# Kernel tuning notes

Hardware: AMD Instinct MI355X
Metric: run time of the kernel (lower is better)

The kernel has to match this reference:

```python
import jax, jax.numpy as jnp
from jax import lax
import numpy as np

B, N, C = 4, 16384, 64
M_POINT, K_SAMPLE = 1024, 32
RADIUS = 0.5
LN_EPS = 1e-5
CP = C + 3  # grouped channels with use_xyz


def _fps(xyz, m):
    """D-FPS: furthest point sampling on Euclidean coords. xyz (B,N,3) -> (B,m) int32."""
    b, n, _ = xyz.shape
    min_d = jnp.full((b, n), 1e10, xyz.dtype)
    pt0 = xyz[:, 0]  # CUDA FPS starts from index 0

    def step(carry, _):
        md, last = carry
        d = jnp.sum((xyz - last[:, None, :]) ** 2, axis=-1)  # (B,N)
        md = jnp.minimum(md, d)
        idx = jnp.argmax(md, axis=1)  # (B,)
        nxt = jnp.take_along_axis(xyz, idx[:, None, None], axis=1)[:, 0]
        return (md, nxt), idx.astype(jnp.int32)

    _, idxs = lax.scan(step, (min_d, pt0), None, length=m - 1)  # (m-1,B)
    return jnp.concatenate([jnp.zeros((1, b), jnp.int32), idxs], axis=0).T  # (B,m)


def _ball_query(xyz, new_xyz, radius, k):
    """First k neighbors (by original index) within radius; pad with first hit. -> (B,M,k)."""
    b, n, _ = xyz.shape
    d2 = jnp.sum((new_xyz[:, :, None, :] - xyz[:, None, :, :]) ** 2, -1)  # (B,M,N)
    scores = jnp.where(d2 <= radius * radius, jnp.arange(n, dtype=jnp.int32), n)
    neg_top, _ = lax.top_k(-scores, k)  # k smallest scores = first k in-radius indices
    idx = -neg_top  # (B,M,k), ascending
    idx = jnp.where(idx < n, idx, idx[..., :1])  # pad invalid slots with first hit
    return idx


def setup_inputs() -> dict:
    key = jax.random.key(0)
    ks = jax.random.split(key, 8)
    points_xyz = jax.random.uniform(ks[0], (B, N, 3)) * 2.0 - 1.0
    features = jax.random.normal(ks[1], (B, C, N))
    prompt_emb = jax.random.normal(ks[2], (1, M_POINT, 2)) * 0.02
    proj_w = jax.random.normal(ks[3], (CP, 2)) * 0.5
    proj_b = jnp.zeros((CP,))
    ln_g = jnp.ones((CP,))
    ln_b = jnp.zeros((CP,))
    pw_w = jax.random.normal(ks[4], (M_POINT, CP)) * 0.05
    pw_b = jnp.zeros((M_POINT,))
    w0 = jax.random.normal(ks[5], (128, CP)) / np.sqrt(CP)
    b0 = jnp.zeros((128,))
    w1 = jax.random.normal(ks[6], (256, 128)) / np.sqrt(128.0)
    b1 = jnp.zeros((256,))
    return dict(points_xyz=points_xyz, features=features, prompt_emb=prompt_emb,
                proj_w=proj_w, proj_b=proj_b, ln_g=ln_g, ln_b=ln_b,
                pw_w=pw_w, pw_b=pw_b, w0=w0, b0=b0, w1=w1, b1=b1)


def reference(points_xyz, features, prompt_emb, proj_w, proj_b, ln_g, ln_b,
              pw_w, pw_b, w0, b0, w1, b1):
    # sample centers (D-FPS)
    indices = _fps(points_xyz, M_POINT)                                   # (B,M)
    new_xyz = jnp.take_along_axis(points_xyz, indices[:, :, None], axis=1)  # (B,M,3)
    # ball-query grouping + gather
    idx = _ball_query(points_xyz, new_xyz, RADIUS, K_SAMPLE)              # (B,M,K)
    gx = jax.vmap(lambda p, i: p[i])(points_xyz, idx)                     # (B,M,K,3)
    gx = gx - new_xyz[:, :, None, :]                                      # relative xyz
    gf = jax.vmap(lambda f, i: f[:, i])(features, idx)                    # (B,C,M,K)
    g = jnp.concatenate([jnp.transpose(gx, (0, 3, 1, 2)), gf], axis=1)    # (B,C+3,M,K)
    # incorporate_prompt
    emb = g.mean(axis=(-2, -1))                                           # (B,C+3)
    pw = jax.nn.softmax(emb @ pw_w.T + pw_b, axis=1)                      # (B,M)
    pe = prompt_emb @ proj_w.T + proj_b                                   # (1,M,C+3)
    mu = pe.mean(-1, keepdims=True)
    var = ((pe - mu) ** 2).mean(-1, keepdims=True)
    pe = (pe - mu) * lax.rsqrt(var + LN_EPS) * ln_g + ln_b
    pe = jax.nn.gelu(pe, approximate=False)                               # (1,M,C+3)
    g = g + pe[0].T[None, :, :, None] * pw[:, None, :, None]              # (B,C+3,M,K)
    # shared MLP (1x1 conv) + ReLU
    h = jax.nn.relu(jnp.einsum('oc,bcmk->bomk', w0, g) + b0[:, None, None])
    h = jax.nn.relu(jnp.einsum('oc,bcmk->bomk', w1, h) + b1[:, None, None])
    # max pool over neighbors K
    pooled = h.max(axis=-1)                                               # (B,256,M)
    return new_xyz, pooled, indices
```

## Files before the change

kernel.cpp:

```cpp
#include <hip/hip_runtime.h>
#include <hip/hip_bf16.h>

#define NB   4
#define NPTS 16384
#define NC   64
#define NM   1024
#define NK   32
#define NCP  67
#define RAD2 0.25f

#define OFF_W0T     0u
#define OFF_W1T     8576u
#define OFF_NEWXYZ  41344u
#define OFF_IDXBALL 53632u
#define OFF_CNT     184704u
#define OFF_EMB     250240u
#define OFF_PW      250624u
#define OFF_PE      254720u
#define OFF_SX      323328u
#define OFF_SY      388864u
#define OFF_SZ      454400u
#define OFF_SKLO    519936u

#define OUT_NEWXYZ 0u
#define OUT_POOLED 12288u
#define OUT_IDX    1060864u

__global__ __launch_bounds__(256) void k_prepw(const float* __restrict__ w0,
                                               const float* __restrict__ w1,
                                               float* __restrict__ w0t,
                                               float* __restrict__ w1t) {
  int t = blockIdx.x * 256 + threadIdx.x;
  if (t < 128 * NCP) { int o = t / NCP, c = t % NCP; w0t[c * 128 + o] = w0[t]; }
  if (t < 256 * 128) { int o2 = t / 128, o = t % 128; w1t[o * 256 + o2] = w1[t]; }
}

__device__ __forceinline__ unsigned mpart3(unsigned v) {
  return (v & 1u) | ((v & 2u) << 2) | ((v & 4u) << 4);
}
__device__ __forceinline__ unsigned cellof(float x, float y, float z) {
  unsigned qx = (unsigned)fminf(fmaxf((x + 1.0f) * 4.0f, 0.0f), 7.0f);
  unsigned qy = (unsigned)fminf(fmaxf((y + 1.0f) * 4.0f, 0.0f), 7.0f);
  unsigned qz = (unsigned)fminf(fmaxf((z + 1.0f) * 4.0f, 0.0f), 7.0f);
  return mpart3(qx) | (mpart3(qy) << 1) | (mpart3(qz) << 2);
}

__global__ __launch_bounds__(1024) void k_sort(const float* __restrict__ xyz,
                                               float* __restrict__ sx,
                                               float* __restrict__ sy,
                                               float* __restrict__ sz,
                                               unsigned* __restrict__ sklo) {
  const int b = blockIdx.x, t = threadIdx.x;
  const int lane = t & 63, wid = t >> 6;
  const float* xb = xyz + (size_t)b * NPTS * 3;
  __shared__ unsigned s_hist[512], s_off[512], s_wsum[8];
  if (t < 512) s_hist[t] = 0u;
  __syncthreads();
#pragma unroll
  for (int i = 0; i < 16; ++i) {
    int p = t + 1024 * i;
    float x = xb[p * 3 + 0], y = xb[p * 3 + 1], z = xb[p * 3 + 2];
    atomicAdd(&s_hist[cellof(x, y, z)], 1u);
  }
  __syncthreads();
  unsigned v = (t < 512) ? s_hist[t] : 0u;
#pragma unroll
  for (int off = 1; off < 64; off <<= 1) {
    unsigned u = __shfl_up(v, off);
    if (lane >= off) v += u;
  }
  if (t < 512 && lane == 63) s_wsum[wid] = v;
  __syncthreads();
  if (t < 512) {
    unsigned add = 0;
    for (int w = 0; w < wid; ++w) add += s_wsum[w];
    s_off[t] = add + v - s_hist[t];
  }
  __syncthreads();
#pragma unroll
  for (int i = 0; i < 16; ++i) {
    int p = t + 1024 * i;
    float x = xb[p * 3 + 0], y = xb[p * 3 + 1], z = xb[p * 3 + 2];
    unsigned pos = atomicAdd(&s_off[cellof(x, y, z)], 1u);
    sx[b * NPTS + pos] = x;
    sy[b * NPTS + pos] = y;
    sz[b * NPTS + pos] = z;
    sklo[b * NPTS + pos] = 16383u - (unsigned)p;
  }
}

__device__ __forceinline__ unsigned long long umax64(unsigned long long a,
                                                     unsigned long long b) {
  return a > b ? a : b;
}

__global__ __launch_bounds__(1024) void k_fps(const float* __restrict__ xyz,
                                              const float* __restrict__ sx,
                                              const float* __restrict__ sy,
                                              const float* __restrict__ sz,
                                              const unsigned* __restrict__ sklo,
                                              float* __restrict__ newxyz,
                                              float* __restrict__ out) {
  const int b = blockIdx.x, t = threadIdx.x;
  const int lane = t & 63, wid = t >> 6;
  const float* xb = xyz + (size_t)b * NPTS * 3;
  const float* bx = sx + b * NPTS;
  const float* by_ = sy + b * NPTS;
  const float* bz_ = sz + b * NPTS;
  const unsigned* bk = sklo + b * NPTS;
  __shared__ float s_md[NPTS];
  __shared__ unsigned short s_klo[NPTS];
  __shared__ float s_bbox[256][6];
  __shared__ unsigned long long s_bkey[256];
  __shared__ int s_list[2][256];
  __shared__ int s_cnt[2];
#pragma unroll
  for (int i = 0; i < 16; ++i) {
    int p = t + 1024 * i;
    s_md[p] = 1e10f;
    s_klo[p] = (unsigned short)bk[p];
  }
  if (t < 256) s_bkey[t] = ((unsigned long long)__float_as_uint(1e10f)) << 32;
  if (t < 2) s_cnt[t] = 0;
  for (int bb = wid; bb < 256; bb += 16) {
    int p = bb * 64 + lane;
    float x = bx[p], y = by_[p], z = bz_[p];
    float xl = x, xh = x, yl = y, yh = y, zl = z, zh = z;
#pragma unroll
    for (int off = 1; off < 64; off <<= 1) {
      xl = fminf(xl, __shfl_xor(xl, off)); xh = fmaxf(xh, __shfl_xor(xh, off));
      yl = fminf(yl, __shfl_xor(yl, off)); yh = fmaxf(yh, __shfl_xor(yh, off));
      zl = fminf(zl, __shfl_xor(zl, off)); zh = fmaxf(zh, __shfl_xor(zh, off));
    }
    if (lane == 0) {
      s_bbox[bb][0] = xl; s_bbox[bb][1] = xh;
      s_bbox[bb][2] = yl; s_bbox[bb][3] = yh;
      s_bbox[bb][4] = zl; s_bbox[bb][5] = zh;
    }
  }
  float lx = xb[0], ly = xb[1], lz = xb[2];
  if (t == 0) {
    newxyz[(size_t)b * NM * 3 + 0] = lx;
    newxyz[(size_t)b * NM * 3 + 1] = ly;
    newxyz[(size_t)b * NM * 3 + 2] = lz;
    out[OUT_NEWXYZ + (size_t)b * NM * 3 + 0] = lx;
    out[OUT_NEWXYZ + (size_t)b * NM * 3 + 1] = ly;
    out[OUT_NEWXYZ + (size_t)b * NM * 3 + 2] = lz;
    out[OUT_IDX + b * NM] = 0.0f;
  }
  __syncthreads();
  for (int s = 1; s < NM; ++s) {
    const int pp = s & 1;
    if (t == 256) s_cnt[pp ^ 1] = 0;
    if (t < 256) {
      float mm = __uint_as_float((unsigned)(s_bkey[t] >> 32));
      float gx = fmaxf(fmaxf(__fsub_rn(s_bbox[t][0], lx), __fsub_rn(lx, s_bbox[t][1])), 0.0f);
      float gy = fmaxf(fmaxf(__fsub_rn(s_bbox[t][2], ly), __fsub_rn(ly, s_bbox[t][3])), 0.0f);
      float gz = fmaxf(fmaxf(__fsub_rn(s_bbox[t][4], lz), __fsub_rn(lz, s_bbox[t][5])), 0.0f);
      float lb = __fadd_rn(__fadd_rn(__fmul_rn(gx, gx), __fmul_rn(gy, gy)),
                           __fmul_rn(gz, gz));
      if (!(lb * 0.999984741f > mm * 1.000015259f)) {
        int pos = atomicAdd(&s_cnt[pp], 1);
        s_list[pp][pos] = t;
      }
    }
    __syncthreads();
    const int nb = s_cnt[pp];
    for (int w = wid; w < nb; w += 16) {
      int bb = s_list[pp][w];
      int p = bb * 64 + lane;
      float dx = __fsub_rn(bx[p], lx);
      float dy = __fsub_rn(by_[p], ly);
      float dz = __fsub_rn(bz_[p], lz);
      float d2 = __fadd_rn(__fadd_rn(__fmul_rn(dx, dx), __fmul_rn(dy, dy)),
                           __fmul_rn(dz, dz));
      float m0 = fminf(s_md[p], d2);
      s_md[p] = m0;
      unsigned long long key =
          (((unsigned long long)__float_as_uint(m0)) << 32) |
          (unsigned long long)s_klo[p];
#pragma unroll
      for (int off = 1; off < 64; off <<= 1) {
        unsigned long long o = __shfl_xor(key, off);
        key = o > key ? o : key;
      }
      if (lane == 0) s_bkey[bb] = key;
    }
    __syncthreads();
    unsigned long long k =
        umax64(umax64(s_bkey[lane], s_bkey[lane + 64]),
               umax64(s_bkey[lane + 128], s_bkey[lane + 192]));
#pragma unroll
    for (int off = 1; off < 64; off <<= 1) {
      unsigned long long o = __shfl_xor(k, off);
      k = o > k ? o : k;
    }
    const int bi = 16383 - (int)(unsigned)(k & 0xffffffffull);
    lx = xb[bi * 3 + 0];
    ly = xb[bi * 3 + 1];
    lz = xb[bi * 3 + 2];
    if (t == 0) {
      newxyz[((size_t)b * NM + s) * 3 + 0] = lx;
      newxyz[((size_t)b * NM + s) * 3 + 1] = ly;
      newxyz[((size_t)b * NM + s) * 3 + 2] = lz;
      out[OUT_NEWXYZ + ((size_t)b * NM + s) * 3 + 0] = lx;
      out[OUT_NEWXYZ + ((size_t)b * NM + s) * 3 + 1] = ly;
      out[OUT_NEWXYZ + ((size_t)b * NM + s) * 3 + 2] = lz;
      out[OUT_IDX + b * NM + s] = (float)bi;
    }
  }
}

__global__ __launch_bounds__(256) void k_ball(const float* __restrict__ xyz,
                                              const float* __restrict__ newxyz,
                                              int* __restrict__ idxball,
                                              int* __restrict__ cnt,
                                              float* __restrict__ emb) {
  __shared__ int s_idx[4][NK];
  const int lane = threadIdx.x & 63, wid = threadIdx.x >> 6;
  const int gid = blockIdx.x * 4 + wid;
  const int b = gid >> 10;
  const float* xb = xyz + (size_t)b * NPTS * 3;
  const float cx = newxyz[gid * 3 + 0];
  const float cy = newxyz[gid * 3 + 1];
  const float cz = newxyz[gid * 3 + 2];
  int total = 0;
  for (int base = 0; base < NPTS && total < NK; base += 64) {
    int n = base + lane;
    float dx = __fsub_rn(xb[n * 3 + 0], cx);
    float dy = __fsub_rn(xb[n * 3 + 1], cy);
    float dz = __fsub_rn(xb[n * 3 + 2], cz);
    float d2 = __fadd_rn(__fadd_rn(__fmul_rn(dx, dx), __fmul_rn(dy, dy)),
                         __fmul_rn(dz, dz));
    bool hit = d2 <= RAD2;
    unsigned long long mask = __ballot(hit);
    int pos = total + (int)__popcll(mask & ((1ull << lane) - 1ull));
    if (hit && pos < NK) s_idx[wid][pos] = n;
    total += (int)__popcll(mask);
  }
  int tt = total < NK ? total : NK;
  if (lane >= tt && lane < NK) s_idx[wid][lane] = s_idx[wid][0];
  int v = 0;
  if (lane < NK) {
    v = s_idx[wid][lane];
    idxball[(size_t)gid * NK + lane] = v;
    atomicAdd(&cnt[b * NPTS + v], 1);
  }
  float sx = 0.f, sy = 0.f, sz = 0.f;
  if (lane < NK) { sx = xb[v * 3 + 0]; sy = xb[v * 3 + 1]; sz = xb[v * 3 + 2]; }
#pragma unroll
  for (int off = 1; off < 64; off <<= 1) {
    sx += __shfl_xor(sx, off);
    sy += __shfl_xor(sy, off);
    sz += __shfl_xor(sz, off);
  }
  if (lane == 0) {
    atomicAdd(&emb[b * 96 + 0], sx - 32.0f * cx);
    atomicAdd(&emb[b * 96 + 1], sy - 32.0f * cy);
    atomicAdd(&emb[b * 96 + 2], sz - 32.0f * cz);
  }
}

__global__ __launch_bounds__(256) void k_embfeat(const float* __restrict__ feat,
                                                 const int* __restrict__ cnt,
                                                 float* __restrict__ emb) {
  const int c = blockIdx.x, b = blockIdx.y;
  const float* f = feat + ((size_t)b * NC + c) * NPTS;
  const int* ct = cnt + b * NPTS;
  float acc = 0.f;
  for (int n = threadIdx.x; n < NPTS; n += 256)
    acc = fmaf((float)ct[n], f[n], acc);
  __shared__ float red[4];
#pragma unroll
  for (int off = 1; off < 64; off <<= 1) acc += __shfl_xor(acc, off);
  if ((threadIdx.x & 63) == 0) red[threadIdx.x >> 6] = acc;
  __syncthreads();
  if (threadIdx.x == 0)
    emb[b * 96 + 3 + c] = red[0] + red[1] + red[2] + red[3];
}

__global__ __launch_bounds__(64) void k_pe(const float* __restrict__ prompt,
                                           const float* __restrict__ projw,
                                           const float* __restrict__ projb,
                                           const float* __restrict__ lng,
                                           const float* __restrict__ lnb,
                                           float* __restrict__ pe) {
  const int m = blockIdx.x, lane = threadIdx.x;
  const float p0 = prompt[m * 2 + 0], p1 = prompt[m * 2 + 1];
  const int c1 = lane, c2 = lane + 64;
  float v1 = p0 * projw[c1 * 2 + 0] + p1 * projw[c1 * 2 + 1] + projb[c1];
  float v2 = 0.f;
  if (c2 < NCP) v2 = p0 * projw[c2 * 2 + 0] + p1 * projw[c2 * 2 + 1] + projb[c2];
  float s = v1 + ((c2 < NCP) ? v2 : 0.f);
#pragma unroll
  for (int off = 1; off < 64; off <<= 1) s += __shfl_xor(s, off);
  float mu = s * (1.0f / 67.0f);
  float d1 = v1 - mu;
  float d2v = (c2 < NCP) ? (v2 - mu) : 0.f;
  float q = d1 * d1 + d2v * d2v;
#pragma unroll
  for (int off = 1; off < 64; off <<= 1) q += __shfl_xor(q, off);
  float inv = 1.0f / sqrtf(q * (1.0f / 67.0f) + 1e-5f);
  {
    float y = d1 * inv * lng[c1] + lnb[c1];
    pe[m * NCP + c1] = 0.5f * y * (1.0f + erff(y * 0.70710678118654752f));
  }
  if (c2 < NCP) {
    float y = (v2 - mu) * inv * lng[c2] + lnb[c2];
    pe[m * NCP + c2] = 0.5f * y * (1.0f + erff(y * 0.70710678118654752f));
  }
}

__global__ __launch_bounds__(1024) void k_pw(const float* __restrict__ emb,
                                             const float* __restrict__ pww,
                                             const float* __restrict__ pwb,
                                             float* __restrict__ pw) {
  const int b = blockIdx.x, m = threadIdx.x;
  __shared__ float se[NCP];
  __shared__ float red[16];
  __shared__ float bcast;
  if (m < NCP) se[m] = emb[b * 96 + m] * (1.0f / 32768.0f);
  __syncthreads();
  float acc = pwb[m];
  for (int c = 0; c < NCP; ++c) acc = fmaf(se[c], pww[m * NCP + c], acc);
  float mx = acc;
#pragma unroll
  for (int off = 1; off < 64; off <<= 1) mx = fmaxf(mx, __shfl_xor(mx, off));
  if ((m & 63) == 0) red[m >> 6] = mx;
  __syncthreads();
  if (m == 0) {
    float v = red[0];
    for (int w = 1; w < 16; ++w) v = fmaxf(v, red[w]);
    bcast = v;
  }
  __syncthreads();
  float e = expf(acc - bcast);
  float ssum = e;
#pragma unroll
  for (int off = 1; off < 64; off <<= 1) ssum += __shfl_xor(ssum, off);
  if ((m & 63) == 0) red[m >> 6] = ssum;
  __syncthreads();
  if (m == 0) {
    float v = 0.f;
    for (int w = 0; w < 16; ++w) v += red[w];
    bcast = v;
  }
  __syncthreads();
  pw[b * NM + m] = e / bcast;
}

__global__ __launch_bounds__(256) void k_main(const float* __restrict__ feat,
                                              const float* __restrict__ xyz,
                                              const float* __restrict__ newxyz,
                                              const int* __restrict__ idxball,
                                              const float* __restrict__ pe,
                                              const float* __restrict__ pwbuf,
                                              const float* __restrict__ w0t,
                                              const float* __restrict__ b0,
                                              const float* __restrict__ w1t,
                                              const float* __restrict__ b1,
                                              float* __restrict__ out) {
  __shared__ __align__(16) float g[NCP * 36];
  __shared__ __align__(16) float h0[128 * 36];
  __shared__ int s_idx[NK];
  __shared__ float spe[NCP];
  const int bid = blockIdx.x;
  const int b = bid >> 10, m = bid & 1023;
  const int t = threadIdx.x;
  const float pwv = pwbuf[bid];
  if (t < NK) {
    int n = idxball[(size_t)bid * NK + t];
    n = n < 0 ? 0 : (n > NPTS - 1 ? NPTS - 1 : n);
    s_idx[t] = n;
  }
  if (t < NCP) spe[t] = pe[m * NCP + t] * pwv;
  __syncthreads();
  for (int e = t; e < NK * NC; e += 256) {
    int k = e >> 6, c = e & 63;
    int n = s_idx[k];
    g[(3 + c) * 36 + k] = feat[((size_t)b * NC + c) * NPTS + n] + spe[3 + c];
  }
  if (t < 96) {
    int k = t & 31, d = t >> 5;
    int n = s_idx[k];
    float cv = newxyz[bid * 3 + d];
    g[d * 36 + k] = (xyz[((size_t)b * NPTS + n) * 3 + d] - cv) + spe[d];
  }
  __syncthreads();
  {
    const int o = t & 127, kb = (t >> 7) * 16;
    float acc[16];
    float bb = b0[o];
#pragma unroll
    for (int j = 0; j < 16; ++j) acc[j] = bb;
    for (int c = 0; c < NCP; ++c) {
      float w = w0t[c * 128 + o];
      const float4* gp = reinterpret_cast<const float4*>(&g[c * 36 + kb]);
#pragma unroll
      for (int qq = 0; qq < 4; ++qq) {
        float4 gv = gp[qq];
        acc[qq * 4 + 0] = fmaf(w, gv.x, acc[qq * 4 + 0]);
        acc[qq * 4 + 1] = fmaf(w, gv.y, acc[qq * 4 + 1]);
        acc[qq * 4 + 2] = fmaf(w, gv.z, acc[qq * 4 + 2]);
        acc[qq * 4 + 3] = fmaf(w, gv.w, acc[qq * 4 + 3]);
      }
    }
    float4* hp = reinterpret_cast<float4*>(&h0[o * 36 + kb]);
#pragma unroll
    for (int qq = 0; qq < 4; ++qq) {
      float4 hv;
      hv.x = fmaxf(acc[qq * 4 + 0], 0.f);
      hv.y = fmaxf(acc[qq * 4 + 1], 0.f);
      hv.z = fmaxf(acc[qq * 4 + 2], 0.f);
      hv.w = fmaxf(acc[qq * 4 + 3], 0.f);
      hp[qq] = hv;
    }
  }
  __syncthreads();
  {
    const int o2 = t;
    float acc[32];
    float bb = b1[o2];
#pragma unroll
    for (int j = 0; j < 32; ++j) acc[j] = bb;
    for (int o = 0; o < 128; ++o) {
      float w = w1t[o * 256 + o2];
      const float4* hp = reinterpret_cast<const float4*>(&h0[o * 36]);
#pragma unroll
      for (int qq = 0; qq < 8; ++qq) {
        float4 hv = hp[qq];
        acc[qq * 4 + 0] = fmaf(w, hv.x, acc[qq * 4 + 0]);
        acc[qq * 4 + 1] = fmaf(w, hv.y, acc[qq * 4 + 1]);
        acc[qq * 4 + 2] = fmaf(w, hv.z, acc[qq * 4 + 2]);
        acc[qq * 4 + 3] = fmaf(w, hv.w, acc[qq * 4 + 3]);
      }
    }
    float mx = 0.f;
#pragma unroll
    for (int k = 0; k < 32; ++k) mx = fmaxf(mx, acc[k]);
    out[OUT_POOLED + ((size_t)(b * 256 + o2)) * NM + m] = mx;
  }
}

extern "C" void kernel_launch(void* const* d_in, const int* in_sizes, int n_in,
                              void* d_out, int out_size, void* d_ws, size_t ws_size,
                              hipStream_t stream) {
  const float* xyz    = (const float*)d_in[0];
  const float* feat   = (const float*)d_in[1];
  const float* prompt = (const float*)d_in[2];
  const float* projw  = (const float*)d_in[3];
  const float* projb  = (const float*)d_in[4];
  const float* lng    = (const float*)d_in[5];
  const float* lnb    = (const float*)d_in[6];
  const float* pww    = (const float*)d_in[7];
  const float* pwb    = (const float*)d_in[8];
  const float* w0     = (const float*)d_in[9];
  const float* b0     = (const float*)d_in[10];
  const float* w1     = (const float*)d_in[11];
  const float* b1     = (const float*)d_in[12];
  float* ws = (float*)d_ws;
  float* out = (float*)d_out;

  float* w0t      = ws + OFF_W0T;
  float* w1t      = ws + OFF_W1T;
  float* nxyz     = ws + OFF_NEWXYZ;
  int*   idxball  = (int*)(ws + OFF_IDXBALL);
  int*   cnt      = (int*)(ws + OFF_CNT);
  float* emb      = ws + OFF_EMB;
  float* pwv      = ws + OFF_PW;
  float* pev      = ws + OFF_PE;
  float* sxw      = ws + OFF_SX;
  float* syw      = ws + OFF_SY;
  float* szw      = ws + OFF_SZ;
  unsigned* sklo  = (unsigned*)(ws + OFF_SKLO);

  hipMemsetAsync(cnt, 0, NB * NPTS * sizeof(int), stream);
  hipMemsetAsync(emb, 0, NB * 96 * sizeof(float), stream);

  k_prepw<<<128, 256, 0, stream>>>(w0, w1, w0t, w1t);
  k_sort<<<NB, 1024, 0, stream>>>(xyz, sxw, syw, szw, sklo);
  k_fps<<<NB, 1024, 0, stream>>>(xyz, sxw, syw, szw, sklo, nxyz, out);
  k_ball<<<NB * NM / 4, 256, 0, stream>>>(xyz, nxyz, idxball, cnt, emb);
  k_embfeat<<<dim3(NC, NB), 256, 0, stream>>>(feat, cnt, emb);
  k_pe<<<NM, 64, 0, stream>>>(prompt, projw, projb, lng, lnb, pev);
  k_pw<<<NB, 1024, 0, stream>>>(emb, pww, pwb, pwv);
  k_main<<<NB * NM, 256, 0, stream>>>(feat, xyz, nxyz, idxball, pev, pwv,
                                      w0t, b0, w1t, b1, out);
}
```

Before: 2.248 ms.

## Restructure FPS loop: one barrier per step, per-wave bucket ownership, cached winner coords

```diff
diff --git a/kernel.cpp b/kernel.cpp
--- a/kernel.cpp
+++ b/kernel.cpp
@@ -93,51 +93,123 @@
                                                      unsigned long long b) {
   return a > b ? a : b;
 }
-
-__global__ __launch_bounds__(1024) void k_fps(const float* __restrict__ xyz,
-                                              const float* __restrict__ sx,
-                                              const float* __restrict__ sy,
-                                              const float* __restrict__ sz,
-                                              const unsigned* __restrict__ sklo,
-                                              float* __restrict__ newxyz,
-                                              float* __restrict__ out) {
+__device__ __forceinline__ unsigned long long pack_key(float m, unsigned kl,
+                                                       int bb) {
+  return (((unsigned long long)__float_as_uint(m)) << 22) |
+         (((unsigned long long)kl) << 8) | (unsigned long long)(unsigned)bb;
+}
+
+template <bool INIT>
+__device__ __forceinline__ void fps_bucket(
+    int bbp, int gl, float lx, float ly, float lz,
+    const float* __restrict__ bx, const float* __restrict__ by,
+    const float* __restrict__ bz, const unsigned* __restrict__ bk,
+    float* s_md, unsigned short* s_klo,
+    unsigned long long* skey_out, float4* swin_out,
+    float* s_bxl, float* s_bxh, float* s_byl, float* s_byh,
+    float* s_bzl, float* s_bzh) {
+  const int p0 = bbp * 64 + gl * 8;
+  float4 xa = *(const float4*)(bx + p0);
+  float4 xc = *(const float4*)(bx + p0 + 4);
+  float4 ya = *(const float4*)(by + p0);
+  float4 yc = *(const float4*)(by + p0 + 4);
+  float4 za = *(const float4*)(bz + p0);
+  float4 zc = *(const float4*)(bz + p0 + 4);
+  float xx[8] = {xa.x, xa.y, xa.z, xa.w, xc.x, xc.y, xc.z, xc.w};
+  float yy[8] = {ya.x, ya.y, ya.z, ya.w, yc.x, yc.y, yc.z, yc.w};
+  float zz[8] = {za.x, za.y, za.z, za.w, zc.x, zc.y, zc.z, zc.w};
+  unsigned kls[8];
+  float mds[8];
+  if constexpr (INIT) {
+    uint4 k0 = *(const uint4*)(bk + p0);
+    uint4 k1 = *(const uint4*)(bk + p0 + 4);
+    kls[0] = k0.x; kls[1] = k0.y; kls[2] = k0.z; kls[3] = k0.w;
+    kls[4] = k1.x; kls[5] = k1.y; kls[6] = k1.z; kls[7] = k1.w;
+  } else {
+    uint4 kv = *(const uint4*)(&s_klo[p0]);
+    kls[0] = kv.x & 0xFFFFu; kls[1] = kv.x >> 16;
+    kls[2] = kv.y & 0xFFFFu; kls[3] = kv.y >> 16;
+    kls[4] = kv.z & 0xFFFFu; kls[5] = kv.z >> 16;
+    kls[6] = kv.w & 0xFFFFu; kls[7] = kv.w >> 16;
+    float4 ma = *(const float4*)(&s_md[p0]);
+    float4 mb = *(const float4*)(&s_md[p0 + 4]);
+    mds[0] = ma.x; mds[1] = ma.y; mds[2] = ma.z; mds[3] = ma.w;
+    mds[4] = mb.x; mds[5] = mb.y; mds[6] = mb.z; mds[7] = mb.w;
+  }
+  unsigned long long best = 0ull;
+  float bwx = 0.f, bwy = 0.f, bwz = 0.f;
+  float nmd[8];
+#pragma unroll
+  for (int i = 0; i < 8; ++i) {
+    float dx = __fsub_rn(xx[i], lx);
+    float dy = __fsub_rn(yy[i], ly);
+    float dz = __fsub_rn(zz[i], lz);
+    float d2 = __fadd_rn(__fadd_rn(__fmul_rn(dx, dx), __fmul_rn(dy, dy)),
+                         __fmul_rn(dz, dz));
+    float m = INIT ? d2 : fminf(mds[i], d2);
+    nmd[i] = m;
+    unsigned long long key = pack_key(m, kls[i], bbp);
+    if (key > best) { best = key; bwx = xx[i]; bwy = yy[i]; bwz = zz[i]; }
+  }
+  *(float4*)(&s_md[p0])     = make_float4(nmd[0], nmd[1], nmd[2], nmd[3]);
+  *(float4*)(&s_md[p0 + 4]) = make_float4(nmd[4], nmd[5], nmd[6], nmd[7]);
+  if constexpr (INIT) {
+    uint4 kw;
+    kw.x = kls[0] | (kls[1] << 16); kw.y = kls[2] | (kls[3] << 16);
+    kw.z = kls[4] | (kls[5] << 16); kw.w = kls[6] | (kls[7] << 16);
+    *(uint4*)(&s_klo[p0]) = kw;
+  }
+  unsigned long long gk = best;
+#pragma unroll
+  for (int off = 1; off < 8; off <<= 1) {
+    unsigned long long o = __shfl_xor(gk, off);
+    gk = o > gk ? o : gk;
+  }
+  if constexpr (INIT) {
+    float xl = xx[0], xh = xx[0], yl = yy[0], yh = yy[0], zl = zz[0], zh = zz[0];
+#pragma unroll
+    for (int i = 1; i < 8; ++i) {
+      xl = fminf(xl, xx[i]); xh = fmaxf(xh, xx[i]);
+      yl = fminf(yl, yy[i]); yh = fmaxf(yh, yy[i]);
+      zl = fminf(zl, zz[i]); zh = fmaxf(zh, zz[i]);
+    }
+#pragma unroll
+    for (int off = 1; off < 8; off <<= 1) {
+      xl = fminf(xl, __shfl_xor(xl, off)); xh = fmaxf(xh, __shfl_xor(xh, off));
+      yl = fminf(yl, __shfl_xor(yl, off)); yh = fmaxf(yh, __shfl_xor(yh, off));
+      zl = fminf(zl, __shfl_xor(zl, off)); zh = fmaxf(zh, __shfl_xor(zh, off));
+    }
+    if (gl == 0) {
+      s_bxl[bbp] = xl; s_bxh[bbp] = xh;
+      s_byl[bbp] = yl; s_byh[bbp] = yh;
+      s_bzl[bbp] = zl; s_bzh[bbp] = zh;
+    }
+  }
+  if (best == gk) swin_out[bbp] = make_float4(bwx, bwy, bwz, 0.f);
+  if (gl == 0) skey_out[bbp] = gk;
+}
+
+__global__ __launch_bounds__(512) void k_fps(const float* __restrict__ xyz,
+                                             const float* __restrict__ sx,
+                                             const float* __restrict__ sy,
+                                             const float* __restrict__ sz,
+                                             const unsigned* __restrict__ sklo,
+                                             float* __restrict__ newxyz,
+                                             float* __restrict__ out) {
   const int b = blockIdx.x, t = threadIdx.x;
-  const int lane = t & 63, wid = t >> 6;
+  const int lane = t & 63, w = t >> 6;
+  const int gl = lane & 7, g = lane >> 3;
   const float* xb = xyz + (size_t)b * NPTS * 3;
   const float* bx = sx + b * NPTS;
-  const float* by_ = sy + b * NPTS;
-  const float* bz_ = sz + b * NPTS;
+  const float* by = sy + b * NPTS;
+  const float* bz = sz + b * NPTS;
   const unsigned* bk = sklo + b * NPTS;
   __shared__ float s_md[NPTS];
   __shared__ unsigned short s_klo[NPTS];
-  __shared__ float s_bbox[256][6];
-  __shared__ unsigned long long s_bkey[256];
-  __shared__ int s_list[2][256];
-  __shared__ int s_cnt[2];
-#pragma unroll
-  for (int i = 0; i < 16; ++i) {
-    int p = t + 1024 * i;
-    s_md[p] = 1e10f;
-    s_klo[p] = (unsigned short)bk[p];
-  }
-  if (t < 256) s_bkey[t] = ((unsigned long long)__float_as_uint(1e10f)) << 32;
-  if (t < 2) s_cnt[t] = 0;
-  for (int bb = wid; bb < 256; bb += 16) {
-    int p = bb * 64 + lane;
-    float x = bx[p], y = by_[p], z = bz_[p];
-    float xl = x, xh = x, yl = y, yh = y, zl = z, zh = z;
-#pragma unroll
-    for (int off = 1; off < 64; off <<= 1) {
-      xl = fminf(xl, __shfl_xor(xl, off)); xh = fmaxf(xh, __shfl_xor(xh, off));
-      yl = fminf(yl, __shfl_xor(yl, off)); yh = fmaxf(yh, __shfl_xor(yh, off));
-      zl = fminf(zl, __shfl_xor(zl, off)); zh = fmaxf(zh, __shfl_xor(zh, off));
-    }
-    if (lane == 0) {
-      s_bbox[bb][0] = xl; s_bbox[bb][1] = xh;
-      s_bbox[bb][2] = yl; s_bbox[bb][3] = yh;
-      s_bbox[bb][4] = zl; s_bbox[bb][5] = zh;
-    }
-  }
+  __shared__ float s_bxl[256], s_bxh[256], s_byl[256], s_byh[256],
+                   s_bzl[256], s_bzh[256];
+  __shared__ unsigned long long s_bkey[2][256];
+  __shared__ float4 s_bwin[2][256];
   float lx = xb[0], ly = xb[1], lz = xb[2];
   if (t == 0) {
     newxyz[(size_t)b * NM * 3 + 0] = lx;
@@ -148,66 +220,68 @@
     out[OUT_NEWXYZ + (size_t)b * NM * 3 + 2] = lz;
     out[OUT_IDX + b * NM] = 0.0f;
   }
+#pragma unroll
+  for (int r = 0; r < 4; ++r) {
+    int bbp = 32 * w + r * 8 + g;
+    fps_bucket<true>(bbp, gl, lx, ly, lz, bx, by, bz, bk, s_md, s_klo,
+                     s_bkey[0], s_bwin[0],
+                     s_bxl, s_bxh, s_byl, s_byh, s_bzl, s_bzh);
+  }
   __syncthreads();
   for (int s = 1; s < NM; ++s) {
-    const int pp = s & 1;
-    if (t == 256) s_cnt[pp ^ 1] = 0;
-    if (t < 256) {
-      float mm = __uint_as_float((unsigned)(s_bkey[t] >> 32));
-      float gx = fmaxf(fmaxf(__fsub_rn(s_bbox[t][0], lx), __fsub_rn(lx, s_bbox[t][1])), 0.0f);
-      float gy = fmaxf(fmaxf(__fsub_rn(s_bbox[t][2], ly), __fsub_rn(ly, s_bbox[t][3])), 0.0f);
-      float gz = fmaxf(fmaxf(__fsub_rn(s_bbox[t][4], lz), __fsub_rn(lz, s_bbox[t][5])), 0.0f);
-      float lb = __fadd_rn(__fadd_rn(__fmul_rn(gx, gx), __fmul_rn(gy, gy)),
-                           __fmul_rn(gz, gz));
-      if (!(lb * 0.999984741f > mm * 1.000015259f)) {
-        int pos = atomicAdd(&s_cnt[pp], 1);
-        s_list[pp][pos] = t;
-      }
-    }
-    __syncthreads();
-    const int nb = s_cnt[pp];
-    for (int w = wid; w < nb; w += 16) {
-      int bb = s_list[pp][w];
-      int p = bb * 64 + lane;
-      float dx = __fsub_rn(bx[p], lx);
-      float dy = __fsub_rn(by_[p], ly);
-      float dz = __fsub_rn(bz_[p], lz);
-      float d2 = __fadd_rn(__fadd_rn(__fmul_rn(dx, dx), __fmul_rn(dy, dy)),
-                           __fmul_rn(dz, dz));
-      float m0 = fminf(s_md[p], d2);
-      s_md[p] = m0;
-      unsigned long long key =
-          (((unsigned long long)__float_as_uint(m0)) << 32) |
-          (unsigned long long)s_klo[p];
-#pragma unroll
-      for (int off = 1; off < 64; off <<= 1) {
-        unsigned long long o = __shfl_xor(key, off);
-        key = o > key ? o : key;
-      }
-      if (lane == 0) s_bkey[bb] = key;
-    }
-    __syncthreads();
+    const int cur = s & 1, prv = cur ^ 1;
     unsigned long long k =
-        umax64(umax64(s_bkey[lane], s_bkey[lane + 64]),
-               umax64(s_bkey[lane + 128], s_bkey[lane + 192]));
+        umax64(umax64(s_bkey[prv][lane], s_bkey[prv][lane + 64]),
+               umax64(s_bkey[prv][lane + 128], s_bkey[prv][lane + 192]));
 #pragma unroll
     for (int off = 1; off < 64; off <<= 1) {
       unsigned long long o = __shfl_xor(k, off);
       k = o > k ? o : k;
     }
-    const int bi = 16383 - (int)(unsigned)(k & 0xffffffffull);
-    lx = xb[bi * 3 + 0];
-    ly = xb[bi * 3 + 1];
-    lz = xb[bi * 3 + 2];
+    const int bbw = (int)(k & 0xFFull);
+    float4 wv = s_bwin[prv][bbw];
+    lx = wv.x; ly = wv.y; lz = wv.z;
     if (t == 0) {
+      const int idx = 16383 - (int)((k >> 8) & 0x3FFFull);
       newxyz[((size_t)b * NM + s) * 3 + 0] = lx;
       newxyz[((size_t)b * NM + s) * 3 + 1] = ly;
       newxyz[((size_t)b * NM + s) * 3 + 2] = lz;
       out[OUT_NEWXYZ + ((size_t)b * NM + s) * 3 + 0] = lx;
       out[OUT_NEWXYZ + ((size_t)b * NM + s) * 3 + 1] = ly;
       out[OUT_NEWXYZ + ((size_t)b * NM + s) * 3 + 2] = lz;
-      out[OUT_IDX + b * NM + s] = (float)bi;
-    }
+      out[OUT_IDX + b * NM + s] = (float)idx;
+    }
+    bool keep = false;
+    if (lane < 32) {
+      const int bbj = 32 * w + lane;
+      unsigned long long kj = s_bkey[prv][bbj];
+      float mm = __uint_as_float((unsigned)(kj >> 22));
+      float gx = fmaxf(fmaxf(__fsub_rn(s_bxl[bbj], lx), __fsub_rn(lx, s_bxh[bbj])), 0.f);
+      float gy = fmaxf(fmaxf(__fsub_rn(s_byl[bbj], ly), __fsub_rn(ly, s_byh[bbj])), 0.f);
+      float gz = fmaxf(fmaxf(__fsub_rn(s_bzl[bbj], lz), __fsub_rn(lz, s_bzh[bbj])), 0.f);
+      float lb = __fadd_rn(__fadd_rn(__fmul_rn(gx, gx), __fmul_rn(gy, gy)),
+                           __fmul_rn(gz, gz));
+      keep = !(__fmul_rn(lb, 0.999984741f) > __fmul_rn(mm, 1.000015259f));
+      if (!keep) {
+        s_bkey[cur][bbj] = kj;
+        s_bwin[cur][bbj] = s_bwin[prv][bbj];
+      }
+    }
+    unsigned long long mask = __ballot(keep);
+    while (mask) {
+      unsigned long long m2 = mask;
+#pragma unroll
+      for (int r = 0; r < 7; ++r) if (r < g) m2 &= (m2 - 1ull);
+      if (m2) {
+        int jj = (int)__builtin_ctzll(m2);
+        fps_bucket<false>(32 * w + jj, gl, lx, ly, lz, bx, by, bz, bk,
+                          s_md, s_klo, s_bkey[cur], s_bwin[cur],
+                          s_bxl, s_bxh, s_byl, s_byh, s_bzl, s_bzh);
+      }
+#pragma unroll
+      for (int r = 0; r < 8; ++r) mask &= (mask - 1ull);
+    }
+    __syncthreads();
   }
 }
 
@@ -479,7 +553,7 @@
 
   k_prepw<<<128, 256, 0, stream>>>(w0, w1, w0t, w1t);
   k_sort<<<NB, 1024, 0, stream>>>(xyz, sxw, syw, szw, sklo);
-  k_fps<<<NB, 1024, 0, stream>>>(xyz, sxw, syw, szw, sklo, nxyz, out);
+  k_fps<<<NB, 512, 0, stream>>>(xyz, sxw, syw, szw, sklo, nxyz, out);
   k_ball<<<NB * NM / 4, 256, 0, stream>>>(xyz, nxyz, idxball, cnt, emb);
   k_embfeat<<<dim3(NC, NB), 256, 0, stream>>>(feat, cnt, emb);
   k_pe<<<NM, 64, 0, stream>>>(prompt, projw, projb, lng, lnb, pev);
```

Result: slower. 2.433 ms (+8.2%).
